# Performance work log

Measured on AMD Instinct MI355X. Metric: run time of the kernel, lower is better.

The kernel has to match this reference:

```python
import jax, jax.numpy as jnp
import numpy as np

N_NODES = 100_000
N_EDGES = 3_200_000
F_IN = 64
HID = 16
N_CLASSES = 4


def setup_inputs() -> dict:
    key = jax.random.key(0)
    ks = jax.random.split(key, 9)
    x = jax.random.normal(ks[0], (N_NODES, F_IN), dtype=jnp.float32)
    edge_index = jax.random.randint(ks[1], (2, N_EDGES), 0, N_NODES, dtype=jnp.int64)
    edge_weight = jax.random.uniform(ks[2], (N_EDGES,), dtype=jnp.float32)
    # Glorot-style init for the three GCN layer weights, zero bias (PyG default)
    W1 = jax.random.normal(ks[3], (F_IN, HID), dtype=jnp.float32) * (1.0 / np.sqrt(F_IN))
    b1 = jnp.zeros((HID,), jnp.float32)
    W3 = jax.random.normal(ks[4], (HID, HID), dtype=jnp.float32) * (1.0 / np.sqrt(HID))
    b3 = jnp.zeros((HID,), jnp.float32)
    W2 = jax.random.normal(ks[5], (HID, N_CLASSES), dtype=jnp.float32) * (1.0 / np.sqrt(HID))
    b2 = jnp.zeros((N_CLASSES,), jnp.float32)
    return {"x": x, "edge_index": edge_index, "edge_weight": edge_weight,
            "W1": W1, "b1": b1, "W3": W3, "b3": b3, "W2": W2, "b2": b2}


def reference(x, edge_index, edge_weight, W1, b1, W3, b3, W2, b2):
    n = x.shape[0]
    # GCNConv default: add self-loops with weight 1, symmetric deg^-1/2 norm
    loop = jnp.arange(n, dtype=edge_index.dtype)
    row = jnp.concatenate([edge_index[0], loop])  # source nodes
    col = jnp.concatenate([edge_index[1], loop])  # target nodes
    ew = jnp.concatenate([edge_weight, jnp.ones((n,), edge_weight.dtype)])
    deg = jax.ops.segment_sum(ew, col, num_segments=n)
    dinv = jnp.where(deg > 0, jax.lax.rsqrt(deg), 0.0)
    norm = dinv[row] * ew * dinv[col]  # [E+N]

    def gcn_conv(h, W, b):
        h = h @ W                                  # [N, out] small matmul first
        msg = norm[:, None] * h[row]               # gather + scale, [E+N, out]
        return jax.ops.segment_sum(msg, col, num_segments=n) + b

    h = jax.nn.relu(gcn_conv(x, W1, b1))
    # dropout is identity in eval mode (training=False)
    h = jax.nn.relu(gcn_conv(h, W3, b3))
    h = gcn_conv(h, W2, b2)
    return jax.nn.log_softmax(h, axis=1)
```

## Files before the change

### kernel.cpp

```cpp
#include <hip/hip_runtime.h>
#include <math.h>

#define NN 100000
#define NE 3200000
#define F_IN 64
#define HID 16
#define NC 4

#define SZB 200
#define NB 500
#define CAP 7424
#define CH 8192
#define NCH 391
#define NW 16

typedef _Float16 half_t;
typedef _Float16 h4f __attribute__((ext_vector_type(4)));

__device__ __forceinline__ unsigned bdiv(unsigned c) {
    return (unsigned)(((unsigned long long)c * 167773ull) >> 25);
}

__device__ __forceinline__ float upw(int pk) {
    unsigned short us = (unsigned short)(pk & 0x7fff);
    half_t h;
    __builtin_memcpy(&h, &us, 2);
    return (float)h;
}

__global__ __launch_bounds__(1024) void k_bin(const int* __restrict__ row,
                                              const int* __restrict__ col,
                                              const float* __restrict__ ew,
                                              int* __restrict__ cursor,
                                              unsigned* __restrict__ bpk,
                                              unsigned char* __restrict__ bcl) {
    __shared__ int h[NB];
    __shared__ int lstart[NB + 1];
    __shared__ int gbase[NB];
    __shared__ int ps[512];
    __shared__ unsigned spk[CH];
    __shared__ unsigned char scl[CH];
    int tid = threadIdx.x;
    for (int i = tid; i < NB; i += 1024) h[i] = 0;
    __syncthreads();
    int e0 = blockIdx.x * CH;
    int e1 = min(e0 + CH, NE);
    int eCnt = e1 - e0;
    for (int i = e0 + tid * 4; i < e1; i += 1024 * 4) {
        int4 c4 = *(const int4*)(col + i);
        atomicAdd(&h[bdiv(c4.x)], 1);
        atomicAdd(&h[bdiv(c4.y)], 1);
        atomicAdd(&h[bdiv(c4.z)], 1);
        atomicAdd(&h[bdiv(c4.w)], 1);
    }
    __syncthreads();
    int c0 = (tid < NB) ? h[tid] : 0;
    if (tid < 512) ps[tid] = c0;
    for (int off = 1; off < 512; off <<= 1) {
        __syncthreads();
        int v = (tid < 512 && tid >= off) ? ps[tid - off] : 0;
        __syncthreads();
        if (tid < 512) ps[tid] += v;
    }
    __syncthreads();
    if (tid < NB) {
        int ex = ps[tid] - c0;
        lstart[tid] = ex;
        h[tid] = ex;
        if (c0) gbase[tid] = tid * CAP + atomicAdd(&cursor[tid], c0);
    }
    if (tid == 0) lstart[NB] = eCnt;
    __syncthreads();
    for (int i = e0 + tid * 4; i < e1; i += 1024 * 4) {
        int4 c4 = *(const int4*)(col + i);
        int4 r4 = *(const int4*)(row + i);
        float4 w4 = *(const float4*)(ew + i);
        half_t hw0 = (half_t)w4.x, hw1 = (half_t)w4.y, hw2 = (half_t)w4.z, hw3 = (half_t)w4.w;
        unsigned short b0, b1, b2, b3;
        __builtin_memcpy(&b0, &hw0, 2); __builtin_memcpy(&b1, &hw1, 2);
        __builtin_memcpy(&b2, &hw2, 2); __builtin_memcpy(&b3, &hw3, 2);
        int p; unsigned bb;
        bb = bdiv(c4.x); p = atomicAdd(&h[bb], 1);
        spk[p] = ((unsigned)r4.x << 15) | (b0 & 0x7fff); scl[p] = (unsigned char)(c4.x - 200u * bb);
        bb = bdiv(c4.y); p = atomicAdd(&h[bb], 1);
        spk[p] = ((unsigned)r4.y << 15) | (b1 & 0x7fff); scl[p] = (unsigned char)(c4.y - 200u * bb);
        bb = bdiv(c4.z); p = atomicAdd(&h[bb], 1);
        spk[p] = ((unsigned)r4.z << 15) | (b2 & 0x7fff); scl[p] = (unsigned char)(c4.z - 200u * bb);
        bb = bdiv(c4.w); p = atomicAdd(&h[bb], 1);
        spk[p] = ((unsigned)r4.w << 15) | (b3 & 0x7fff); scl[p] = (unsigned char)(c4.w - 200u * bb);
    }
    __syncthreads();
    for (int i = tid; i < eCnt; i += 1024) {
        int lo = 0, hi = NB;
        while (hi - lo > 1) {
            int mid = (lo + hi) >> 1;
            if (lstart[mid] <= i) lo = mid; else hi = mid;
        }
        int d = gbase[lo] + (i - lstart[lo]);
        if (d < (lo + 1) * CAP) {
            bpk[d] = spk[i];
            bcl[d] = scl[i];
        }
    }
}

__global__ __launch_bounds__(1024) void k_sort(const unsigned* __restrict__ bpk,
                                               const unsigned char* __restrict__ bcl,
                                               const int* __restrict__ cursor,
                                               const float* __restrict__ x,
                                               const float* __restrict__ W1,
                                               unsigned* __restrict__ epk,
                                               int2* __restrict__ nodeptr2,
                                               float* __restrict__ dinv,
                                               half_t* __restrict__ tt1) {
    __shared__ int hw[NW][SZB];
    __shared__ int cnt[SZB];
    __shared__ int ps[SZB];
    __shared__ unsigned stage[CAP];
    __shared__ float Ws[F_IN * HID];
    int b = blockIdx.x, tid = threadIdx.x;
    int w = tid >> 6;
    for (int i = tid; i < NW * SZB; i += 1024) ((int*)hw)[i] = 0;
    for (int i = tid; i < F_IN * HID; i += 1024) Ws[i] = W1[i];
    __syncthreads();
    int s = b * CAP;
    int m = min(cursor[b], CAP);
    int e = s + m;
    for (int i = s + tid; i < e; i += 1024)
        atomicAdd(&hw[w][bcl[i]], 1);
    __syncthreads();
    if (tid < SZB) {
        int c = 0;
#pragma unroll
        for (int ww = 0; ww < NW; ww++) c += hw[ww][tid];
        cnt[tid] = c;
    }
    __syncthreads();
    int pc = (tid < SZB) ? ((cnt[tid] + 3) & ~3) : 0;
    if (tid < SZB) ps[tid] = pc;
    for (int off = 1; off < SZB; off <<= 1) {
        __syncthreads();
        int v = (tid < SZB && tid >= off) ? ps[tid - off] : 0;
        __syncthreads();
        if (tid < SZB) ps[tid] += v;
    }
    __syncthreads();
    if (tid < SZB) {
        int run = ps[tid] - pc;
#pragma unroll
        for (int ww = 0; ww < NW; ww++) {
            int t = hw[ww][tid];
            hw[ww][tid] = run;
            run += t;
        }
    }
    __syncthreads();
    int mpad = min(ps[SZB - 1], CAP);
    for (int i = tid; i < mpad; i += 1024) stage[i] = 0u;
    __syncthreads();
    for (int i = s + tid; i < e; i += 1024) {
        int cl = bcl[i];
        int pos = atomicAdd(&hw[w][cl], 1);
        if (pos < CAP) stage[pos] = bpk[i];
    }
    __syncthreads();
    for (int i = tid; i < mpad; i += 1024) epk[s + i] = stage[i];
    int nl = tid >> 2, l = tid & 3;
    float di = 0.0f;
    int n = b * SZB + nl;
    if (nl < SZB) {
        int pcn = (cnt[nl] + 3) & ~3;
        int ex = ps[nl] - pcn;
        float sw = 0.0f;
        for (int i = ex + l; i < ex + pcn; i += 4) sw += upw((int)stage[i]);
        sw += __shfl_xor(sw, 1, 4);
        sw += __shfl_xor(sw, 2, 4);
        di = rsqrtf(1.0f + sw);
        if (n < NN && l == 0) {
            nodeptr2[n] = make_int2(s + ex, s + ex + pcn);
            dinv[n] = di;
        }
    }
    if (nl < SZB && n < NN) {
        float part[HID];
#pragma unroll
        for (int j = 0; j < HID; j++) part[j] = 0.0f;
        const float4* xp = (const float4*)(x + (size_t)n * F_IN) + l * 4;
#pragma unroll
        for (int k4 = 0; k4 < 4; k4++) {
            float4 v = xp[k4];
            int k = l * 16 + k4 * 4;
#pragma unroll
            for (int j = 0; j < HID; j++) {
                part[j] += v.x * Ws[(k + 0) * HID + j];
                part[j] += v.y * Ws[(k + 1) * HID + j];
                part[j] += v.z * Ws[(k + 2) * HID + j];
                part[j] += v.w * Ws[(k + 3) * HID + j];
            }
        }
#pragma unroll
        for (int j = 0; j < HID; j++) {
            part[j] += __shfl_xor(part[j], 1, 4);
            part[j] += __shfl_xor(part[j], 2, 4);
        }
        h4f o;
        o.x = (half_t)(di * part[4 * l + 0]);
        o.y = (half_t)(di * part[4 * l + 1]);
        o.z = (half_t)(di * part[4 * l + 2]);
        o.w = (half_t)(di * part[4 * l + 3]);
        ((h4f*)tt1)[n * 4 + l] = o;
    }
}

template <int DN>
__global__ __launch_bounds__(256) void k_aggf(const unsigned* __restrict__ epk,
                                              const int2* __restrict__ nptr,
                                              const half_t* __restrict__ tt_in,
                                              const float* __restrict__ bias,
                                              const float* __restrict__ dinv,
                                              const float* __restrict__ Wn,
                                              half_t* __restrict__ tt_out) {
    __shared__ float Ws[HID * DN];
    if (threadIdx.x < HID * DN) Ws[threadIdx.x] = Wn[threadIdx.x];
    __syncthreads();
    int tid = blockIdx.x * 256 + threadIdx.x;
    int n = tid >> 2;
    int l = tid & 3;
    if (n >= NN) return;
    int2 p = nptr[n];
    const h4f* ttp = (const h4f*)tt_in;
    h4f sv = ttp[n * 4 + l];
    float ax = 0.f, ay = 0.f, az = 0.f, aw = 0.f;
    for (int base = p.x; base < p.y; base += 4) {
        int4 q = *(const int4*)(epk + base);
        int r0 = ((unsigned)q.x) >> 15;
        int r1 = ((unsigned)q.y) >> 15;
        int r2 = ((unsigned)q.z) >> 15;
        int r3 = ((unsigned)q.w) >> 15;
        float w0 = upw(q.x), w1 = upw(q.y), w2 = upw(q.z), w3 = upw(q.w);
        h4f v0 = ttp[r0 * 4 + l];
        h4f v1 = ttp[r1 * 4 + l];
        h4f v2 = ttp[r2 * 4 + l];
        h4f v3 = ttp[r3 * 4 + l];
        ax += w0 * (float)v0.x; ay += w0 * (float)v0.y; az += w0 * (float)v0.z; aw += w0 * (float)v0.w;
        ax += w1 * (float)v1.x; ay += w1 * (float)v1.y; az += w1 * (float)v1.z; aw += w1 * (float)v1.w;
        ax += w2 * (float)v2.x; ay += w2 * (float)v2.y; az += w2 * (float)v2.z; aw += w2 * (float)v2.w;
        ax += w3 * (float)v3.x; ay += w3 * (float)v3.y; az += w3 * (float)v3.z; aw += w3 * (float)v3.w;
    }
    float di = dinv[n];
    const float4* b4p = (const float4*)bias;
    float4 b4 = b4p[l];
    float hreg[4];
    hreg[0] = fmaxf(b4.x + di * (ax + (float)sv.x), 0.f);
    hreg[1] = fmaxf(b4.y + di * (ay + (float)sv.y), 0.f);
    hreg[2] = fmaxf(b4.z + di * (az + (float)sv.z), 0.f);
    hreg[3] = fmaxf(b4.w + di * (aw + (float)sv.w), 0.f);
    if (DN == 16) {
        float ox = 0.f, oy = 0.f, oz = 0.f, ow = 0.f;
#pragma unroll
        for (int k = 0; k < HID; k++) {
            float hk = __shfl(hreg[k & 3], k >> 2, 4);
            const float4 wk = *(const float4*)&Ws[k * 16 + 4 * l];
            ox += hk * wk.x; oy += hk * wk.y; oz += hk * wk.z; ow += hk * wk.w;
        }
        h4f ov;
        ov.x = (half_t)(di * ox); ov.y = (half_t)(di * oy);
        ov.z = (half_t)(di * oz); ov.w = (half_t)(di * ow);
        ((h4f*)tt_out)[n * 4 + l] = ov;
    } else {
        float o = 0.f;
#pragma unroll
        for (int k = 0; k < HID; k++) {
            float hk = __shfl(hreg[k & 3], k >> 2, 4);
            o += hk * Ws[k * DN + l];
        }
        tt_out[(size_t)n * DN + l] = (half_t)(di * o);
    }
}

__global__ __launch_bounds__(256) void k_agg4sm(const unsigned* __restrict__ epk,
                                                const int2* __restrict__ nptr,
                                                const half_t* __restrict__ tt,
                                                const float* __restrict__ bias,
                                                const float* __restrict__ dinv,
                                                float* __restrict__ out) {
    int tid = blockIdx.x * 256 + threadIdx.x;
    int n = tid >> 2;
    int l = tid & 3;
    if (n >= NN) return;
    int2 p = nptr[n];
    float self = (float)tt[n * 4 + l];
    float acc = 0.f;
    for (int base = p.x; base < p.y; base += 4) {
        int4 q = *(const int4*)(epk + base);
        int r0 = ((unsigned)q.x) >> 15;
        int r1 = ((unsigned)q.y) >> 15;
        int r2 = ((unsigned)q.z) >> 15;
        int r3 = ((unsigned)q.w) >> 15;
        acc += upw(q.x) * (float)tt[r0 * 4 + l];
        acc += upw(q.y) * (float)tt[r1 * 4 + l];
        acc += upw(q.z) * (float)tt[r2 * 4 + l];
        acc += upw(q.w) * (float)tt[r3 * 4 + l];
    }
    float di = dinv[n];
    float logit = bias[l] + di * (acc + self);
    float m = logit;
    m = fmaxf(m, __shfl_xor(m, 1, 4));
    m = fmaxf(m, __shfl_xor(m, 2, 4));
    float ex = expf(logit - m);
    float s = ex;
    s += __shfl_xor(s, 1, 4);
    s += __shfl_xor(s, 2, 4);
    out[n * 4 + l] = logit - m - logf(s);
}

extern "C" void kernel_launch(void* const* d_in, const int* in_sizes, int n_in,
                              void* d_out, int out_size, void* d_ws, size_t ws_size,
                              hipStream_t stream) {
    const float* x  = (const float*)d_in[0];
    const int*   ei = (const int*)d_in[1];
    const float* ew = (const float*)d_in[2];
    const float* W1 = (const float*)d_in[3];
    const float* b1 = (const float*)d_in[4];
    const float* W3 = (const float*)d_in[5];
    const float* b3 = (const float*)d_in[6];
    const float* W2 = (const float*)d_in[7];
    const float* b2 = (const float*)d_in[8];
    float* out = (float*)d_out;

    const int* row = ei;
    const int* col = ei + NE;

    const size_t NEP = (size_t)NB * CAP;
    char* ws = (char*)d_ws;
    size_t off = 0;
    float*         dinv     = (float*)(ws + off);         off += 400000;
    int2*          nodeptr2 = (int2*)(ws + off);          off += 800000;
    int*           cursor   = (int*)(ws + off);           off += 2048;
    unsigned*      epk      = (unsigned*)(ws + off);      off += NEP * 4;
    unsigned*      bpk      = (unsigned*)(ws + off);      off += NEP * 4;
    unsigned char* bcl      = (unsigned char*)(ws + off); off += (NEP + 15) & ~15ull;
    half_t*        tt1      = (half_t*)(ws + off);        off += (size_t)NN * HID * 2;
    half_t*        tt2      = (half_t*)(ws + off);        off += (size_t)NN * HID * 2;
    half_t*        tt3      = (half_t*)(ws + off);        off += (size_t)NN * NC * 2;

    hipMemsetAsync(cursor, 0, NB * sizeof(int), stream);

    k_bin<<<NCH, 1024, 0, stream>>>(row, col, ew, cursor, bpk, bcl);
    k_sort<<<NB, 1024, 0, stream>>>(bpk, bcl, cursor, x, W1, epk, nodeptr2, dinv, tt1);

    int gA = (NN * 4 + 255) / 256;

    k_aggf<HID><<<gA, 256, 0, stream>>>(epk, nodeptr2, tt1, b1, dinv, W3, tt2);
    k_aggf<NC><<<gA, 256, 0, stream>>>(epk, nodeptr2, tt2, b3, dinv, W2, tt3);
    k_agg4sm<<<gA, 256, 0, stream>>>(epk, nodeptr2, tt3, b2, dinv, out);
}
```

Baseline: 223.4 us.

## Use wave-shuffle scans, store bucket ids, and software-pipeline edge gathers

The shared-memory Hillis-Steele scans in the binning and sorting kernels are replaced by wave-level shuffle scans with a small cross-wave combine, which removes many block barriers. The binning kernel now records each staged edge's bucket id in shared memory, so the per-edge binary search over bucket starts is no longer needed during scatter. Both aggregation kernels are software-pipelined: the next packed edge quad and its gathered features are loaded before the current quad is accumulated, to hide gather latency. The cost is extra shared memory for bucket ids and more live registers in the aggregation loops.

```diff
diff --git a/kernel.cpp b/kernel.cpp
--- a/kernel.cpp
+++ b/kernel.cpp
@@ -35,12 +35,14 @@
                                               unsigned* __restrict__ bpk,
                                               unsigned char* __restrict__ bcl) {
     __shared__ int h[NB];
-    __shared__ int lstart[NB + 1];
+    __shared__ int lstart[NB];
     __shared__ int gbase[NB];
-    __shared__ int ps[512];
+    __shared__ int wsum[8];
     __shared__ unsigned spk[CH];
+    __shared__ unsigned short sbk[CH];
     __shared__ unsigned char scl[CH];
     int tid = threadIdx.x;
+    int lane = tid & 63, wv = tid >> 6;
     for (int i = tid; i < NB; i += 1024) h[i] = 0;
     __syncthreads();
     int e0 = blockIdx.x * CH;
@@ -55,21 +57,23 @@
     }
     __syncthreads();
     int c0 = (tid < NB) ? h[tid] : 0;
-    if (tid < 512) ps[tid] = c0;
-    for (int off = 1; off < 512; off <<= 1) {
-        __syncthreads();
-        int v = (tid < 512 && tid >= off) ? ps[tid - off] : 0;
-        __syncthreads();
-        if (tid < 512) ps[tid] += v;
-    }
+    int v = c0;
+#pragma unroll
+    for (int off = 1; off < 64; off <<= 1) {
+        int t = __shfl_up(v, off, 64);
+        if (lane >= off) v += t;
+    }
+    if (wv < 8 && lane == 63) wsum[wv] = v;
     __syncthreads();
     if (tid < NB) {
-        int ex = ps[tid] - c0;
+        int pre = 0;
+#pragma unroll
+        for (int ww = 0; ww < 8; ww++) pre += (ww < wv) ? wsum[ww] : 0;
+        int ex = (v + pre) - c0;
         lstart[tid] = ex;
         h[tid] = ex;
         if (c0) gbase[tid] = tid * CAP + atomicAdd(&cursor[tid], c0);
     }
-    if (tid == 0) lstart[NB] = eCnt;
     __syncthreads();
     for (int i = e0 + tid * 4; i < e1; i += 1024 * 4) {
         int4 c4 = *(const int4*)(col + i);
@@ -82,20 +86,20 @@
         int p; unsigned bb;
         bb = bdiv(c4.x); p = atomicAdd(&h[bb], 1);
         spk[p] = ((unsigned)r4.x << 15) | (b0 & 0x7fff); scl[p] = (unsigned char)(c4.x - 200u * bb);
+        sbk[p] = (unsigned short)bb;
         bb = bdiv(c4.y); p = atomicAdd(&h[bb], 1);
         spk[p] = ((unsigned)r4.y << 15) | (b1 & 0x7fff); scl[p] = (unsigned char)(c4.y - 200u * bb);
+        sbk[p] = (unsigned short)bb;
         bb = bdiv(c4.z); p = atomicAdd(&h[bb], 1);
         spk[p] = ((unsigned)r4.z << 15) | (b2 & 0x7fff); scl[p] = (unsigned char)(c4.z - 200u * bb);
+        sbk[p] = (unsigned short)bb;
         bb = bdiv(c4.w); p = atomicAdd(&h[bb], 1);
         spk[p] = ((unsigned)r4.w << 15) | (b3 & 0x7fff); scl[p] = (unsigned char)(c4.w - 200u * bb);
+        sbk[p] = (unsigned short)bb;
     }
     __syncthreads();
     for (int i = tid; i < eCnt; i += 1024) {
-        int lo = 0, hi = NB;
-        while (hi - lo > 1) {
-            int mid = (lo + hi) >> 1;
-            if (lstart[mid] <= i) lo = mid; else hi = mid;
-        }
+        int lo = sbk[i];
         int d = gbase[lo] + (i - lstart[lo]);
         if (d < (lo + 1) * CAP) {
             bpk[d] = spk[i];
@@ -116,9 +120,11 @@
     __shared__ int hw[NW][SZB];
     __shared__ int cnt[SZB];
     __shared__ int ps[SZB];
+    __shared__ int wsum4[4];
     __shared__ unsigned stage[CAP];
     __shared__ float Ws[F_IN * HID];
     int b = blockIdx.x, tid = threadIdx.x;
+    int lane = tid & 63;
     int w = tid >> 6;
     for (int i = tid; i < NW * SZB; i += 1024) ((int*)hw)[i] = 0;
     for (int i = tid; i < F_IN * HID; i += 1024) Ws[i] = W1[i];
@@ -137,12 +143,19 @@
     }
     __syncthreads();
     int pc = (tid < SZB) ? ((cnt[tid] + 3) & ~3) : 0;
-    if (tid < SZB) ps[tid] = pc;
-    for (int off = 1; off < SZB; off <<= 1) {
-        __syncthreads();
-        int v = (tid < SZB && tid >= off) ? ps[tid - off] : 0;
-        __syncthreads();
-        if (tid < SZB) ps[tid] += v;
+    int v = pc;
+#pragma unroll
+    for (int off = 1; off < 64; off <<= 1) {
+        int t = __shfl_up(v, off, 64);
+        if (lane >= off) v += t;
+    }
+    if (w < 4 && lane == 63) wsum4[w] = v;
+    __syncthreads();
+    if (tid < SZB) {
+        int pre = 0;
+#pragma unroll
+        for (int ww = 0; ww < 4; ww++) pre += (ww < w) ? wsum4[ww] : 0;
+        ps[tid] = v + pre;
     }
     __syncthreads();
     if (tid < SZB) {
@@ -188,14 +201,14 @@
         const float4* xp = (const float4*)(x + (size_t)n * F_IN) + l * 4;
 #pragma unroll
         for (int k4 = 0; k4 < 4; k4++) {
-            float4 v = xp[k4];
+            float4 vx = xp[k4];
             int k = l * 16 + k4 * 4;
 #pragma unroll
             for (int j = 0; j < HID; j++) {
-                part[j] += v.x * Ws[(k + 0) * HID + j];
-                part[j] += v.y * Ws[(k + 1) * HID + j];
-                part[j] += v.z * Ws[(k + 2) * HID + j];
-                part[j] += v.w * Ws[(k + 3) * HID + j];
+                part[j] += vx.x * Ws[(k + 0) * HID + j];
+                part[j] += vx.y * Ws[(k + 1) * HID + j];
+                part[j] += vx.z * Ws[(k + 2) * HID + j];
+                part[j] += vx.w * Ws[(k + 3) * HID + j];
             }
         }
 #pragma unroll
@@ -211,6 +224,19 @@
         ((h4f*)tt1)[n * 4 + l] = o;
     }
 }
+
+#define ACC4(Q, V0, V1, V2, V3)                                                 \
+    do {                                                                        \
+        float w0 = upw((Q).x), w1 = upw((Q).y), w2 = upw((Q).z), w3 = upw((Q).w); \
+        ax += w0 * (float)(V0).x; ay += w0 * (float)(V0).y;                     \
+        az += w0 * (float)(V0).z; aw += w0 * (float)(V0).w;                     \
+        ax += w1 * (float)(V1).x; ay += w1 * (float)(V1).y;                     \
+        az += w1 * (float)(V1).z; aw += w1 * (float)(V1).w;                     \
+        ax += w2 * (float)(V2).x; ay += w2 * (float)(V2).y;                     \
+        az += w2 * (float)(V2).z; aw += w2 * (float)(V2).w;                     \
+        ax += w3 * (float)(V3).x; ay += w3 * (float)(V3).y;                     \
+        az += w3 * (float)(V3).z; aw += w3 * (float)(V3).w;                     \
+    } while (0)
 
 template <int DN>
 __global__ __launch_bounds__(256) void k_aggf(const unsigned* __restrict__ epk,
@@ -231,21 +257,31 @@
     const h4f* ttp = (const h4f*)tt_in;
     h4f sv = ttp[n * 4 + l];
     float ax = 0.f, ay = 0.f, az = 0.f, aw = 0.f;
-    for (int base = p.x; base < p.y; base += 4) {
+    int base = p.x;
+    const int pend = p.y;
+    if (base < pend) {
         int4 q = *(const int4*)(epk + base);
-        int r0 = ((unsigned)q.x) >> 15;
-        int r1 = ((unsigned)q.y) >> 15;
-        int r2 = ((unsigned)q.z) >> 15;
-        int r3 = ((unsigned)q.w) >> 15;
-        float w0 = upw(q.x), w1 = upw(q.y), w2 = upw(q.z), w3 = upw(q.w);
-        h4f v0 = ttp[r0 * 4 + l];
-        h4f v1 = ttp[r1 * 4 + l];
-        h4f v2 = ttp[r2 * 4 + l];
-        h4f v3 = ttp[r3 * 4 + l];
-        ax += w0 * (float)v0.x; ay += w0 * (float)v0.y; az += w0 * (float)v0.z; aw += w0 * (float)v0.w;
-        ax += w1 * (float)v1.x; ay += w1 * (float)v1.y; az += w1 * (float)v1.z; aw += w1 * (float)v1.w;
-        ax += w2 * (float)v2.x; ay += w2 * (float)v2.y; az += w2 * (float)v2.z; aw += w2 * (float)v2.w;
-        ax += w3 * (float)v3.x; ay += w3 * (float)v3.y; az += w3 * (float)v3.z; aw += w3 * (float)v3.w;
+        base += 4;
+        bool more = base < pend;
+        int4 qn = *(const int4*)(epk + (more ? base : p.x));
+        h4f v0 = ttp[((((unsigned)q.x) >> 15) << 2) + l];
+        h4f v1 = ttp[((((unsigned)q.y) >> 15) << 2) + l];
+        h4f v2 = ttp[((((unsigned)q.z) >> 15) << 2) + l];
+        h4f v3 = ttp[((((unsigned)q.w) >> 15) << 2) + l];
+        while (more) {
+            base += 4;
+            bool more2 = base < pend;
+            int4 qnn = *(const int4*)(epk + (more2 ? base : p.x));
+            h4f u0 = ttp[((((unsigned)qn.x) >> 15) << 2) + l];
+            h4f u1 = ttp[((((unsigned)qn.y) >> 15) << 2) + l];
+            h4f u2 = ttp[((((unsigned)qn.z) >> 15) << 2) + l];
+            h4f u3 = ttp[((((unsigned)qn.w) >> 15) << 2) + l];
+            ACC4(q, v0, v1, v2, v3);
+            q = qn; qn = qnn;
+            v0 = u0; v1 = u1; v2 = u2; v3 = u3;
+            more = more2;
+        }
+        ACC4(q, v0, v1, v2, v3);
     }
     float di = dinv[n];
     const float4* b4p = (const float4*)bias;
@@ -291,27 +327,48 @@
     int2 p = nptr[n];
     float self = (float)tt[n * 4 + l];
     float acc = 0.f;
-    for (int base = p.x; base < p.y; base += 4) {
+    int base = p.x;
+    const int pend = p.y;
+    if (base < pend) {
         int4 q = *(const int4*)(epk + base);
-        int r0 = ((unsigned)q.x) >> 15;
-        int r1 = ((unsigned)q.y) >> 15;
-        int r2 = ((unsigned)q.z) >> 15;
-        int r3 = ((unsigned)q.w) >> 15;
-        acc += upw(q.x) * (float)tt[r0 * 4 + l];
-        acc += upw(q.y) * (float)tt[r1 * 4 + l];
-        acc += upw(q.z) * (float)tt[r2 * 4 + l];
-        acc += upw(q.w) * (float)tt[r3 * 4 + l];
+        base += 4;
+        bool more = base < pend;
+        int4 qn = *(const int4*)(epk + (more ? base : p.x));
+        float v0 = (float)tt[((((unsigned)q.x) >> 15) << 2) + l];
+        float v1 = (float)tt[((((unsigned)q.y) >> 15) << 2) + l];
+        float v2 = (float)tt[((((unsigned)q.z) >> 15) << 2) + l];
+        float v3 = (float)tt[((((unsigned)q.w) >> 15) << 2) + l];
+        while (more) {
+            base += 4;
+            bool more2 = base < pend;
+            int4 qnn = *(const int4*)(epk + (more2 ? base : p.x));
+            float u0 = (float)tt[((((unsigned)qn.x) >> 15) << 2) + l];
+            float u1 = (float)tt[((((unsigned)qn.y) >> 15) << 2) + l];
+            float u2 = (float)tt[((((unsigned)qn.z) >> 15) << 2) + l];
+            float u3 = (float)tt[((((unsigned)qn.w) >> 15) << 2) + l];
+            acc += upw(q.x) * v0;
+            acc += upw(q.y) * v1;
+            acc += upw(q.z) * v2;
+            acc += upw(q.w) * v3;
+            q = qn; qn = qnn;
+            v0 = u0; v1 = u1; v2 = u2; v3 = u3;
+            more = more2;
+        }
+        acc += upw(q.x) * v0;
+        acc += upw(q.y) * v1;
+        acc += upw(q.z) * v2;
+        acc += upw(q.w) * v3;
     }
     float di = dinv[n];
     float logit = bias[l] + di * (acc + self);
-    float m = logit;
-    m = fmaxf(m, __shfl_xor(m, 1, 4));
-    m = fmaxf(m, __shfl_xor(m, 2, 4));
-    float ex = expf(logit - m);
-    float s = ex;
-    s += __shfl_xor(s, 1, 4);
-    s += __shfl_xor(s, 2, 4);
-    out[n * 4 + l] = logit - m - logf(s);
+    float mx = logit;
+    mx = fmaxf(mx, __shfl_xor(mx, 1, 4));
+    mx = fmaxf(mx, __shfl_xor(mx, 2, 4));
+    float ex = expf(logit - mx);
+    float sm = ex;
+    sm += __shfl_xor(sm, 1, 4);
+    sm += __shfl_xor(sm, 2, 4);
+    out[n * 4 + l] = logit - mx - logf(sm);
 }
 
 extern "C" void kernel_launch(void* const* d_in, const int* in_sizes, int n_in,
```

After: 220.9 us. No clear change (-1.1%).
